# Performance work log

Hardware: AMD Instinct MI355X
Metric: run time of the kernel (lower is better)

The kernel has to match this reference:

```python
import jax, jax.numpy as jnp
import numpy as np

EMB = 256
VOCAB = 50000
STEPS = 100  # max extra decode iterations after the first (output rows = 101)
BN_EPS = 1e-5


def setup_inputs() -> dict:
    key = jax.random.key(0)
    ks = jax.random.split(key, 10)
    s = 0.05
    return {
        "board": jax.random.normal(ks[0], (19, 19), jnp.float32),
        "conv_w": jax.random.normal(ks[1], (1, 1, 3, 3), jnp.float32) * s,
        "conv_b": jnp.zeros((1,), jnp.float32),
        "bn_gamma": jnp.ones((1,), jnp.float32),
        "bn_beta": jnp.zeros((1,), jnp.float32),
        "p": jnp.ones((8,), jnp.float32),
        "W_lin": jax.random.normal(ks[2], (EMB, 361), jnp.float32) * s,
        "b_lin": jnp.zeros((EMB,), jnp.float32),
        "W_ih": jax.random.normal(ks[3], (4 * EMB, EMB), jnp.float32) * s,
        "b_ih": jnp.zeros((4 * EMB,), jnp.float32),
        "W_hh": jax.random.normal(ks[4], (4 * EMB, EMB), jnp.float32) * s,
        "b_hh": jnp.zeros((4 * EMB,), jnp.float32),
        "W_dec": jax.random.normal(ks[5], (VOCAB, EMB), jnp.float32) * s,
        "b_dec": jnp.zeros((VOCAB,), jnp.float32),
    }


def reference(board, conv_w, conv_b, bn_gamma, bn_beta, p,
              W_lin, b_lin, W_ih, b_ih, W_hh, b_hh, W_dec, b_dec):
    # --- shared conv + batchnorm (training-mode stats), all 8 "layers" share weights ---
    def conv_bn(x):  # x: [1,1,19,19]
        y = jax.lax.conv_general_dilated(x, conv_w, (1, 1), 'SAME') + conv_b.reshape(1, 1, 1, 1)
        mu = y.mean()
        var = jnp.mean((y - mu) ** 2)  # biased var over N,H,W (C=1)
        return bn_gamma[0] * (y - mu) * jax.lax.rsqrt(var + BN_EPS) + bn_beta[0]

    relu = jax.nn.relu
    x = board.reshape(1, 1, 19, 19)
    d1 = relu(p[0] * conv_bn(x))
    d2 = d1
    for i in (1, 3, 5):  # fixed structural unroll (residual pairs)
        d1 = relu(p[i] * conv_bn(d1))
        d1 = d2 = relu(p[i + 1] * conv_bn(d1) + d2)
    d1 = relu(conv_bn(d1))  # cnn_list[7], no scalar

    feat = W_lin @ d1.reshape(361) + b_lin  # [EMB]

    # --- LSTMCell (PyTorch gate order i,f,g,o) ---
    def cell(x_in, h, c):
        gates = W_ih @ x_in + b_ih + W_hh @ h + b_hh  # [4*EMB]
        i, f, g, o = jnp.split(gates, 4)
        c2 = jax.nn.sigmoid(f) * c + jax.nn.sigmoid(i) * jnp.tanh(g)
        h2 = jax.nn.sigmoid(o) * jnp.tanh(c2)
        return h2, c2

    zeros = jnp.zeros((EMB,), feat.dtype)
    h, c = cell(feat, zeros, zeros)
    logit0 = W_dec @ h + b_dec  # [VOCAB]

    # (original breaks early on argmax==3; max output rows = 101)
    def step(carry, _):
        h, c = carry
        h2, c2 = cell(h, h, c)
        return (h2, c2), W_dec @ h2 + b_dec

    _, logits = jax.lax.scan(step, (h, c), None, length=STEPS)  # [STEPS, VOCAB]
    out = jax.nn.relu(jnp.concatenate([logit0[None, :], logits], axis=0))  # [101, VOCAB]
    return out
```

## Files before the change

kernel.cpp:

```cpp
#include <hip/hip_runtime.h>

typedef _Float16 v2h __attribute__((ext_vector_type(2)));
typedef _Float16 v8h __attribute__((ext_vector_type(8)));
typedef float v4f __attribute__((ext_vector_type(4)));

#define EMB 256
#define VOCAB 50000
#define NSTEP 101

__device__ __forceinline__ float sigf(float x) {
    return 1.f / (1.f + __expf(-x));
}
__device__ __forceinline__ float tanhf_(float x) {
    float e = __expf(2.f * fabsf(x));
    float th = 1.f - 2.f / (e + 1.f);
    return copysignf(th, x);
}
__device__ __forceinline__ float fdot2_(v2h a, v2h b, float c) {
    return __builtin_amdgcn_fdot2(a, b, c, false);
}

__global__ __launch_bounds__(384) void k_conv(
        const float* __restrict__ board, const float* __restrict__ conv_w,
        const float* __restrict__ conv_b, const float* __restrict__ gamma,
        const float* __restrict__ beta, const float* __restrict__ p,
        float* __restrict__ d1_out) {
    __shared__ float cur[361];
    __shared__ float red1[8], red2[8];
    __shared__ float stats[2];
    const int t = threadIdx.x;
    const bool act = t < 361;
    const int r = t / 19, c = t % 19;
    float w[9];
#pragma unroll
    for (int k = 0; k < 9; ++k) w[k] = conv_w[k];
    const float cb = conv_b[0], ga = gamma[0], be = beta[0];
    float scales[8] = {p[0], p[1], p[2], p[3], p[4], p[5], p[6], 1.f};
    const int mode[8] = {2, 0, 1, 0, 1, 0, 1, 0};
    if (act) cur[t] = board[t];
    float d2r = 0.f;
    __syncthreads();
#pragma unroll
    for (int it = 0; it < 8; ++it) {
        float y = 0.f;
        if (act) {
#pragma unroll
            for (int di = 0; di < 3; ++di)
#pragma unroll
                for (int dj = 0; dj < 3; ++dj) {
                    int rr = r + di - 1, cc2 = c + dj - 1;
                    if (rr >= 0 && rr < 19 && cc2 >= 0 && cc2 < 19)
                        y += cur[rr * 19 + cc2] * w[di * 3 + dj];
                }
            y += cb;
        }
        float s1 = y, s2 = y * y;
        for (int m = 32; m; m >>= 1) {
            s1 += __shfl_xor(s1, m);
            s2 += __shfl_xor(s2, m);
        }
        const int wv = t >> 6;
        if ((t & 63) == 0) { red1[wv] = s1; red2[wv] = s2; }
        __syncthreads();
        if (t == 0) {
            float a = 0.f, b2 = 0.f;
            for (int i = 0; i < 6; ++i) { a += red1[i]; b2 += red2[i]; }
            float mu = a / 361.f;
            float var = b2 / 361.f - mu * mu;
            stats[0] = mu;
            stats[1] = rsqrtf(var + 1e-5f);
        }
        __syncthreads();
        float mu = stats[0], rs = stats[1];
        float v = ga * (y - mu) * rs + be;
        v *= scales[it];
        if (mode[it] == 1) v += d2r;
        v = fmaxf(v, 0.f);
        if (mode[it] != 0) d2r = v;
        if (act) cur[t] = v;
        __syncthreads();
    }
    if (act) d1_out[t] = cur[t];
}

__global__ __launch_bounds__(256) void k_prep(
        const float* __restrict__ Wlin, const float* __restrict__ blin,
        const float* __restrict__ d1,
        const float* __restrict__ Wih, const float* __restrict__ bih,
        const float* __restrict__ Whh, const float* __restrict__ bhh,
        float* __restrict__ feat, _Float16* __restrict__ wsum,
        float* __restrict__ bsum) {
    const int b = blockIdx.x, t = threadIdx.x;
    if (b < 16) {
        const int r = b * 16 + (t >> 4), kc = t & 15;
        const int k0 = kc * 23, k1 = (k0 + 23 < 361) ? k0 + 23 : 361;
        const float* wrow = Wlin + r * 361;
        float acc = 0.f;
        for (int k = k0; k < k1; ++k) acc += wrow[k] * d1[k];
        for (int m = 1; m < 16; m <<= 1) acc += __shfl_xor(acc, m);
        if (kc == 0) feat[r] = acc + blin[r];
    } else if (b < 80) {
        const int base = (b - 16) * 4096 + t;
#pragma unroll
        for (int i = 0; i < 16; ++i) {
            int idx = base + i * 256;
            wsum[idx] = (_Float16)(Wih[idx] + Whh[idx]);
        }
    } else {
        for (int i = t; i < 1024; i += 256) bsum[i] = bih[i] + bhh[i];
    }
}

__global__ __launch_bounds__(256) void k_gates0(
        const float* __restrict__ Wih, const float* __restrict__ feat,
        const float* __restrict__ bih, const float* __restrict__ bhh,
        float* __restrict__ gates0) {
    const int r = blockIdx.x * 16 + (threadIdx.x >> 4), kc = threadIdx.x & 15;
    const float* wrow = Wih + r * 256 + kc * 16;
    const float* f = feat + kc * 16;
    float acc = 0.f;
#pragma unroll
    for (int k = 0; k < 16; ++k) acc += wrow[k] * f[k];
    for (int m = 1; m < 16; m <<= 1) acc += __shfl_xor(acc, m);
    if (kc == 0) gates0[r] = acc + bih[r] + bhh[r];
}

__global__ __launch_bounds__(512, 2) void k_lstm(
        const _Float16* __restrict__ wsum, const float* __restrict__ bsum,
        const float* __restrict__ gates0, _Float16* __restrict__ Hg) {
    extern __shared__ char smem[];
    _Float16* Wl = (_Float16*)smem;
    _Float16* hbuf = (_Float16*)(smem + 131072);
    float* part = (float*)(smem + 131584);
    const int t = threadIdx.x;
    const int idx = t & 255;
    const int half = t >> 8;
    const int kbase = half * 128;
    const int sw = (t & 15) << 4;

    v2h wr[4][48];
#pragma unroll
    for (int j = 0; j < 4; ++j) {
        const _Float16* src = wsum + (idx + 256 * j) * 256 + kbase;
#pragma unroll
        for (int q = 0; q < 12; ++q) {
            float4 fv = *(const float4*)(src + q * 8);
            const v2h* vp = (const v2h*)&fv;
            wr[j][q * 4 + 0] = vp[0];
            wr[j][q * 4 + 1] = vp[1];
            wr[j][q * 4 + 2] = vp[2];
            wr[j][q * 4 + 3] = vp[3];
        }
    }
#pragma unroll
    for (int j = 0; j < 4; ++j) {
        const _Float16* src = wsum + (idx + 256 * j) * 256 + kbase + 96;
#pragma unroll
        for (int cc = 0; cc < 4; ++cc) {
            float4 fv = *(const float4*)(src + cc * 8);
            const int c = j * 4 + cc;
            *(float4*)((char*)Wl + t * 256 + ((c * 16) ^ sw)) = fv;
        }
    }
    const float bs0 = bsum[idx], bs1 = bsum[idx + 256];
    const float bs2 = bsum[idx + 512], bs3 = bsum[idx + 768];
    float cst = 0.f;
    if (half == 0) {
        float gi = gates0[idx], gg = gates0[idx + 512], go = gates0[idx + 768];
        cst = sigf(gi) * tanhf_(gg);
        float h = sigf(go) * tanhf_(cst);
        hbuf[idx] = (_Float16)h;
        Hg[idx] = (_Float16)h;
    }
    __syncthreads();

    for (int step = 1; step <= 100; ++step) {
        float acc[4];
        acc[0] = 0.f; acc[1] = 0.f; acc[2] = 0.f; acc[3] = 0.f;
        const v2h* hp = ((const v2h*)hbuf) + half * 64;
#pragma unroll
        for (int q = 0; q < 12; ++q) {
            float4 hv = *(const float4*)(hp + q * 4);
            const v2h* h4 = (const v2h*)&hv;
#pragma unroll
            for (int j = 0; j < 4; ++j) {
#pragma unroll
                for (int u = 0; u < 4; ++u)
                    acc[j] = fdot2_(wr[j][q * 4 + u], h4[u], acc[j]);
            }
        }
#pragma unroll
        for (int cc = 0; cc < 4; ++cc) {
            float4 hv = *(const float4*)(hp + 48 + cc * 4);
            const v2h* h4 = (const v2h*)&hv;
#pragma unroll
            for (int j = 0; j < 4; ++j) {
                const int c = j * 4 + cc;
                float4 wv = *(const float4*)((const char*)Wl + t * 256 + ((c * 16) ^ sw));
                const v2h* w4 = (const v2h*)&wv;
#pragma unroll
                for (int u = 0; u < 4; ++u)
                    acc[j] = fdot2_(w4[u], h4[u], acc[j]);
            }
        }
        if (half == 1) {
            part[0 * 256 + idx] = acc[0];
            part[1 * 256 + idx] = acc[1];
            part[2 * 256 + idx] = acc[2];
            part[3 * 256 + idx] = acc[3];
        }
        __syncthreads();
        if (half == 0) {
            float gi = acc[0] + part[0 * 256 + idx] + bs0;
            float gf = acc[1] + part[1 * 256 + idx] + bs1;
            float gg = acc[2] + part[2 * 256 + idx] + bs2;
            float go = acc[3] + part[3 * 256 + idx] + bs3;
            cst = sigf(gf) * cst + sigf(gi) * tanhf_(gg);
            float h = sigf(go) * tanhf_(cst);
            hbuf[idx] = (_Float16)h;
            Hg[step * 256 + idx] = (_Float16)h;
        }
        __syncthreads();
    }
}

__global__ __launch_bounds__(256) void k_gemm(
        const float* __restrict__ Wdec, const float* __restrict__ bdec,
        const _Float16* __restrict__ Hg, float* __restrict__ out) {
    __shared__ _Float16 Hl[112 * 264];
    const int t = threadIdx.x;
    float4 z; z.x = 0.f; z.y = 0.f; z.z = 0.f; z.w = 0.f;
    for (int i = t; i < 3696; i += 256) ((float4*)Hl)[i] = z;
    __syncthreads();
    for (int i = t; i < 101 * 32; i += 256) {
        int row = i >> 5, kc = i & 31;
        float4 v = ((const float4*)Hg)[i];
        *(float4*)(Hl + row * 264 + kc * 8) = v;
    }
    __syncthreads();

    const int l = t & 63, wv = t >> 6;
    const int mrow = blockIdx.x * 64 + wv * 16 + (l & 15);
    const int mcl = (mrow < VOCAB) ? mrow : (VOCAB - 1);
    const float* arow = Wdec + (size_t)mcl * 256 + ((l >> 4) << 3);
    const _Float16* brow = Hl + (l & 15) * 264 + ((l >> 4) << 3);

    v4f acc[7];
#pragma unroll
    for (int nt = 0; nt < 7; ++nt) {
#pragma unroll
        for (int j = 0; j < 4; ++j) acc[nt][j] = 0.f;
    }
#pragma unroll
    for (int ks = 0; ks < 8; ++ks) {
        float4 a0 = *(const float4*)(arow + ks * 32);
        float4 a1 = *(const float4*)(arow + ks * 32 + 4);
        v8h af;
        af[0] = (_Float16)a0.x; af[1] = (_Float16)a0.y;
        af[2] = (_Float16)a0.z; af[3] = (_Float16)a0.w;
        af[4] = (_Float16)a1.x; af[5] = (_Float16)a1.y;
        af[6] = (_Float16)a1.z; af[7] = (_Float16)a1.w;
#pragma unroll
        for (int nt = 0; nt < 7; ++nt) {
            v8h bf = *(const v8h*)(brow + nt * 16 * 264 + ks * 32);
            acc[nt] = __builtin_amdgcn_mfma_f32_16x16x32_f16(af, bf, acc[nt], 0, 0, 0);
        }
    }
    const int rowq = blockIdx.x * 64 + wv * 16 + ((l >> 4) << 2);
    if (rowq < VOCAB) {
        float4 bd = *(const float4*)(bdec + rowq);
#pragma unroll
        for (int nt = 0; nt < 7; ++nt) {
            int tt = nt * 16 + (l & 15);
            if (tt <= 100) {
                float4 v;
                v.x = fmaxf(acc[nt][0] + bd.x, 0.f);
                v.y = fmaxf(acc[nt][1] + bd.y, 0.f);
                v.z = fmaxf(acc[nt][2] + bd.z, 0.f);
                v.w = fmaxf(acc[nt][3] + bd.w, 0.f);
                *(float4*)(out + (size_t)tt * VOCAB + rowq) = v;
            }
        }
    }
}

extern "C" void kernel_launch(void* const* d_in, const int* in_sizes, int n_in,
                              void* d_out, int out_size, void* d_ws, size_t ws_size,
                              hipStream_t stream) {
    const float* board  = (const float*)d_in[0];
    const float* conv_w = (const float*)d_in[1];
    const float* conv_b = (const float*)d_in[2];
    const float* bn_g   = (const float*)d_in[3];
    const float* bn_b   = (const float*)d_in[4];
    const float* p      = (const float*)d_in[5];
    const float* Wlin   = (const float*)d_in[6];
    const float* blin   = (const float*)d_in[7];
    const float* Wih    = (const float*)d_in[8];
    const float* bih    = (const float*)d_in[9];
    const float* Whh    = (const float*)d_in[10];
    const float* bhh    = (const float*)d_in[11];
    const float* Wdec   = (const float*)d_in[12];
    const float* bdec   = (const float*)d_in[13];
    float* out = (float*)d_out;
    char* ws = (char*)d_ws;

    _Float16* wsum  = (_Float16*)(ws);
    _Float16* Hg    = (_Float16*)(ws + 524288);
    float* d1       = (float*)(ws + 576512);
    float* feat     = (float*)(ws + 578560);
    float* gates0   = (float*)(ws + 579584);
    float* bsum     = (float*)(ws + 583680);

    k_conv<<<1, 384, 0, stream>>>(board, conv_w, conv_b, bn_g, bn_b, p, d1);
    k_prep<<<81, 256, 0, stream>>>(Wlin, blin, d1, Wih, bih, Whh, bhh, feat, wsum, bsum);
    k_gates0<<<64, 256, 0, stream>>>(Wih, feat, bih, bhh, gates0);
    k_lstm<<<1, 512, 135680, stream>>>(wsum, bsum, gates0, Hg);
    k_gemm<<<782, 256, 0, stream>>>(Wdec, bdec, Hg, out);
}
```

Before: 304.3 us.

## Overlap W_dec fp16 conversion with LSTM recurrence and fuse prep kernels

Merges the conv/BN, feature, gates0 and weight-sum prep into one kernel and so cuts the launch count from five to three. The LSTM kernel is launched with 128 extra blocks that convert W_dec to fp16 in workspace while block 0 runs the serial recurrence. The recurrence is re-split across 4 threads per gate-row group, reduced with shuffles instead of shared-memory partials, and uses double-buffered h so one barrier per step is dropped. The GEMM then reads half the weight bytes as fp16. This depends on the workspace being large enough and falls back to the fp32 GEMM otherwise. The converter blocks may compete with the recurrence for bandwidth or compute units.

```diff
diff --git a/kernel.cpp b/kernel.cpp
--- a/kernel.cpp
+++ b/kernel.cpp
@@ -1,12 +1,12 @@
 #include <hip/hip_runtime.h>
 
 typedef _Float16 v2h __attribute__((ext_vector_type(2)));
+typedef _Float16 v4h __attribute__((ext_vector_type(4)));
 typedef _Float16 v8h __attribute__((ext_vector_type(8)));
 typedef float v4f __attribute__((ext_vector_type(4)));
 
 #define EMB 256
 #define VOCAB 50000
-#define NSTEP 101
 
 __device__ __forceinline__ float sigf(float x) {
     return 1.f / (1.f + __expf(-x));
@@ -20,182 +20,205 @@
     return __builtin_amdgcn_fdot2(a, b, c, false);
 }
 
-__global__ __launch_bounds__(384) void k_conv(
+__global__ __launch_bounds__(512) void k_pre(
         const float* __restrict__ board, const float* __restrict__ conv_w,
         const float* __restrict__ conv_b, const float* __restrict__ gamma,
         const float* __restrict__ beta, const float* __restrict__ p,
-        float* __restrict__ d1_out) {
-    __shared__ float cur[361];
-    __shared__ float red1[8], red2[8];
-    __shared__ float stats[2];
-    const int t = threadIdx.x;
-    const bool act = t < 361;
-    const int r = t / 19, c = t % 19;
-    float w[9];
-#pragma unroll
-    for (int k = 0; k < 9; ++k) w[k] = conv_w[k];
-    const float cb = conv_b[0], ga = gamma[0], be = beta[0];
-    float scales[8] = {p[0], p[1], p[2], p[3], p[4], p[5], p[6], 1.f};
-    const int mode[8] = {2, 0, 1, 0, 1, 0, 1, 0};
-    if (act) cur[t] = board[t];
-    float d2r = 0.f;
-    __syncthreads();
-#pragma unroll
-    for (int it = 0; it < 8; ++it) {
-        float y = 0.f;
-        if (act) {
-#pragma unroll
-            for (int di = 0; di < 3; ++di)
-#pragma unroll
-                for (int dj = 0; dj < 3; ++dj) {
-                    int rr = r + di - 1, cc2 = c + dj - 1;
-                    if (rr >= 0 && rr < 19 && cc2 >= 0 && cc2 < 19)
-                        y += cur[rr * 19 + cc2] * w[di * 3 + dj];
-                }
-            y += cb;
-        }
-        float s1 = y, s2 = y * y;
-        for (int m = 32; m; m >>= 1) {
-            s1 += __shfl_xor(s1, m);
-            s2 += __shfl_xor(s2, m);
-        }
-        const int wv = t >> 6;
-        if ((t & 63) == 0) { red1[wv] = s1; red2[wv] = s2; }
-        __syncthreads();
-        if (t == 0) {
-            float a = 0.f, b2 = 0.f;
-            for (int i = 0; i < 6; ++i) { a += red1[i]; b2 += red2[i]; }
-            float mu = a / 361.f;
-            float var = b2 / 361.f - mu * mu;
-            stats[0] = mu;
-            stats[1] = rsqrtf(var + 1e-5f);
-        }
-        __syncthreads();
-        float mu = stats[0], rs = stats[1];
-        float v = ga * (y - mu) * rs + be;
-        v *= scales[it];
-        if (mode[it] == 1) v += d2r;
-        v = fmaxf(v, 0.f);
-        if (mode[it] != 0) d2r = v;
-        if (act) cur[t] = v;
-        __syncthreads();
-    }
-    if (act) d1_out[t] = cur[t];
-}
-
-__global__ __launch_bounds__(256) void k_prep(
         const float* __restrict__ Wlin, const float* __restrict__ blin,
-        const float* __restrict__ d1,
         const float* __restrict__ Wih, const float* __restrict__ bih,
         const float* __restrict__ Whh, const float* __restrict__ bhh,
-        float* __restrict__ feat, _Float16* __restrict__ wsum,
-        float* __restrict__ bsum) {
+        _Float16* __restrict__ wsum, float* __restrict__ bsum,
+        float* __restrict__ gates0) {
+    __shared__ float cur[361];
+    __shared__ float feat_s[256];
+    __shared__ float red1[8], red2[8], stats[2];
     const int b = blockIdx.x, t = threadIdx.x;
-    if (b < 16) {
-        const int r = b * 16 + (t >> 4), kc = t & 15;
-        const int k0 = kc * 23, k1 = (k0 + 23 < 361) ? k0 + 23 : 361;
-        const float* wrow = Wlin + r * 361;
-        float acc = 0.f;
-        for (int k = k0; k < k1; ++k) acc += wrow[k] * d1[k];
-        for (int m = 1; m < 16; m <<= 1) acc += __shfl_xor(acc, m);
-        if (kc == 0) feat[r] = acc + blin[r];
-    } else if (b < 80) {
-        const int base = (b - 16) * 4096 + t;
-#pragma unroll
-        for (int i = 0; i < 16; ++i) {
-            int idx = base + i * 256;
+    if (b == 0) {
+        const bool act = t < 361;
+        const int r = t / 19, c = t % 19;
+        float w[9];
+#pragma unroll
+        for (int k = 0; k < 9; ++k) w[k] = conv_w[k];
+        const float cb = conv_b[0], ga = gamma[0], be = beta[0];
+        float scales[8] = {p[0], p[1], p[2], p[3], p[4], p[5], p[6], 1.f};
+        const int mode[8] = {2, 0, 1, 0, 1, 0, 1, 0};
+        if (act) cur[t] = board[t];
+        float d2r = 0.f;
+        __syncthreads();
+#pragma unroll
+        for (int it = 0; it < 8; ++it) {
+            float y = 0.f;
+            if (act) {
+#pragma unroll
+                for (int di = 0; di < 3; ++di)
+#pragma unroll
+                    for (int dj = 0; dj < 3; ++dj) {
+                        int rr = r + di - 1, cc2 = c + dj - 1;
+                        if (rr >= 0 && rr < 19 && cc2 >= 0 && cc2 < 19)
+                            y += cur[rr * 19 + cc2] * w[di * 3 + dj];
+                    }
+                y += cb;
+            }
+            float s1 = y, s2 = y * y;
+            for (int m = 32; m; m >>= 1) {
+                s1 += __shfl_xor(s1, m);
+                s2 += __shfl_xor(s2, m);
+            }
+            const int wv = t >> 6;
+            if ((t & 63) == 0) { red1[wv] = s1; red2[wv] = s2; }
+            __syncthreads();
+            if (t == 0) {
+                float a = 0.f, b2 = 0.f;
+                for (int i = 0; i < 8; ++i) { a += red1[i]; b2 += red2[i]; }
+                float mu = a / 361.f;
+                float var = b2 / 361.f - mu * mu;
+                stats[0] = mu;
+                stats[1] = rsqrtf(var + 1e-5f);
+            }
+            __syncthreads();
+            float mu = stats[0], rs = stats[1];
+            float v = ga * (y - mu) * rs + be;
+            v *= scales[it];
+            if (mode[it] == 1) v += d2r;
+            v = fmaxf(v, 0.f);
+            if (mode[it] != 0) d2r = v;
+            if (act) cur[t] = v;
+            __syncthreads();
+        }
+        {
+            const int fr = t >> 1, fh = t & 1;
+            const int k0 = fh ? 184 : 0, k1 = fh ? 361 : 184;
+            const float* wrow = Wlin + fr * 361;
+            float acc = 0.f;
+            for (int k = k0; k < k1; ++k) acc += wrow[k] * cur[k];
+            acc += __shfl_xor(acc, 1);
+            if (fh == 0) feat_s[fr] = acc + blin[fr];
+        }
+        __syncthreads();
+#pragma unroll
+        for (int rr = 0; rr < 2; ++rr) {
+            const int row = t + rr * 512;
+            const float4* wr4 = (const float4*)(Wih + row * 256);
+            float a = 0.f;
+            for (int k = 0; k < 64; ++k) {
+                float4 wv = wr4[k];
+                float4 fv = *(const float4*)(feat_s + k * 4);
+                a += wv.x * fv.x + wv.y * fv.y + wv.z * fv.z + wv.w * fv.w;
+            }
+            gates0[row] = a + bih[row] + bhh[row];
+        }
+    } else if (b <= 8) {
+        const int base = (b - 1) * 32768 + t;
+#pragma unroll
+        for (int i = 0; i < 64; ++i) {
+            int idx = base + i * 512;
             wsum[idx] = (_Float16)(Wih[idx] + Whh[idx]);
         }
     } else {
-        for (int i = t; i < 1024; i += 256) bsum[i] = bih[i] + bhh[i];
-    }
-}
-
-__global__ __launch_bounds__(256) void k_gates0(
-        const float* __restrict__ Wih, const float* __restrict__ feat,
-        const float* __restrict__ bih, const float* __restrict__ bhh,
-        float* __restrict__ gates0) {
-    const int r = blockIdx.x * 16 + (threadIdx.x >> 4), kc = threadIdx.x & 15;
-    const float* wrow = Wih + r * 256 + kc * 16;
-    const float* f = feat + kc * 16;
-    float acc = 0.f;
-#pragma unroll
-    for (int k = 0; k < 16; ++k) acc += wrow[k] * f[k];
-    for (int m = 1; m < 16; m <<= 1) acc += __shfl_xor(acc, m);
-    if (kc == 0) gates0[r] = acc + bih[r] + bhh[r];
+        for (int i = t; i < 1024; i += 512) bsum[i] = bih[i] + bhh[i];
+    }
 }
 
 __global__ __launch_bounds__(512, 2) void k_lstm(
         const _Float16* __restrict__ wsum, const float* __restrict__ bsum,
-        const float* __restrict__ gates0, _Float16* __restrict__ Hg) {
+        const float* __restrict__ gates0, _Float16* __restrict__ Hg,
+        const float* __restrict__ Wdec, _Float16* __restrict__ wdh) {
+    if (blockIdx.x != 0) {
+        const float4* src = (const float4*)Wdec;
+        const int gid = (blockIdx.x - 1) * 512 + threadIdx.x;
+        for (int i = gid; i < 3200000; i += 65536) {
+            float4 v = src[i];
+            v4h o;
+            o[0] = (_Float16)v.x; o[1] = (_Float16)v.y;
+            o[2] = (_Float16)v.z; o[3] = (_Float16)v.w;
+            *(v4h*)(wdh + (size_t)i * 4) = o;
+        }
+        return;
+    }
     extern __shared__ char smem[];
     _Float16* Wl = (_Float16*)smem;
-    _Float16* hbuf = (_Float16*)(smem + 131072);
-    float* part = (float*)(smem + 131584);
+    char* hb0 = smem + 131072;
     const int t = threadIdx.x;
-    const int idx = t & 255;
-    const int half = t >> 8;
-    const int kbase = half * 128;
+    const int g = t >> 2;
+    const int ks = t & 3;
+    const int k0 = ks * 64;
     const int sw = (t & 15) << 4;
 
-    v2h wr[4][48];
-#pragma unroll
-    for (int j = 0; j < 4; ++j) {
-        const _Float16* src = wsum + (idx + 256 * j) * 256 + kbase;
-#pragma unroll
-        for (int q = 0; q < 12; ++q) {
-            float4 fv = *(const float4*)(src + q * 8);
+    int rows[8];
+#pragma unroll
+    for (int j = 0; j < 4; ++j) { rows[j] = g + 256 * j; rows[j + 4] = g + 128 + 256 * j; }
+
+    v2h wr[8][24];
+#pragma unroll
+    for (int j = 0; j < 8; ++j) {
+        const _Float16* src = wsum + rows[j] * 256 + k0;
+#pragma unroll
+        for (int q6 = 0; q6 < 6; ++q6) {
+            float4 fv = *(const float4*)(src + q6 * 8);
             const v2h* vp = (const v2h*)&fv;
-            wr[j][q * 4 + 0] = vp[0];
-            wr[j][q * 4 + 1] = vp[1];
-            wr[j][q * 4 + 2] = vp[2];
-            wr[j][q * 4 + 3] = vp[3];
-        }
-    }
-#pragma unroll
-    for (int j = 0; j < 4; ++j) {
-        const _Float16* src = wsum + (idx + 256 * j) * 256 + kbase + 96;
-#pragma unroll
-        for (int cc = 0; cc < 4; ++cc) {
+            wr[j][q6 * 4 + 0] = vp[0];
+            wr[j][q6 * 4 + 1] = vp[1];
+            wr[j][q6 * 4 + 2] = vp[2];
+            wr[j][q6 * 4 + 3] = vp[3];
+        }
+    }
+#pragma unroll
+    for (int j = 0; j < 8; ++j)
+#pragma unroll
+        for (int q = 0; q < 24; ++q)
+            asm volatile("" : "+v"(wr[j][q]));
+
+#pragma unroll
+    for (int j = 0; j < 8; ++j) {
+        const _Float16* src = wsum + rows[j] * 256 + k0 + 48;
+#pragma unroll
+        for (int cc = 0; cc < 2; ++cc) {
             float4 fv = *(const float4*)(src + cc * 8);
-            const int c = j * 4 + cc;
+            const int c = j * 2 + cc;
             *(float4*)((char*)Wl + t * 256 + ((c * 16) ^ sw)) = fv;
         }
     }
-    const float bs0 = bsum[idx], bs1 = bsum[idx + 256];
-    const float bs2 = bsum[idx + 512], bs3 = bsum[idx + 768];
+    float bsv[8];
+#pragma unroll
+    for (int j = 0; j < 8; ++j) bsv[j] = bsum[rows[j]];
+
+    const int cell = (ks == 0) ? g : g + 128;
+    const int haddr = ((cell >> 6) * 144) + ((cell & 63) * 2);
     float cst = 0.f;
-    if (half == 0) {
-        float gi = gates0[idx], gg = gates0[idx + 512], go = gates0[idx + 768];
+    if (ks < 2) {
+        float gi = gates0[cell], gg = gates0[cell + 512], go = gates0[cell + 768];
         cst = sigf(gi) * tanhf_(gg);
         float h = sigf(go) * tanhf_(cst);
-        hbuf[idx] = (_Float16)h;
-        Hg[idx] = (_Float16)h;
+        *(_Float16*)(hb0 + haddr) = (_Float16)h;
+        Hg[cell] = (_Float16)h;
     }
     __syncthreads();
 
     for (int step = 1; step <= 100; ++step) {
-        float acc[4];
-        acc[0] = 0.f; acc[1] = 0.f; acc[2] = 0.f; acc[3] = 0.f;
-        const v2h* hp = ((const v2h*)hbuf) + half * 64;
-#pragma unroll
-        for (int q = 0; q < 12; ++q) {
-            float4 hv = *(const float4*)(hp + q * 4);
+        const char* hr = hb0 + ((step + 1) & 1) * 576;
+        char* hw = hb0 + (step & 1) * 576;
+        const char* hsl = hr + ks * 144;
+        float acc[8];
+#pragma unroll
+        for (int j = 0; j < 8; ++j) acc[j] = 0.f;
+#pragma unroll
+        for (int q = 0; q < 6; ++q) {
+            float4 hv = *(const float4*)(hsl + q * 16);
             const v2h* h4 = (const v2h*)&hv;
 #pragma unroll
-            for (int j = 0; j < 4; ++j) {
+            for (int j = 0; j < 8; ++j) {
 #pragma unroll
                 for (int u = 0; u < 4; ++u)
                     acc[j] = fdot2_(wr[j][q * 4 + u], h4[u], acc[j]);
             }
         }
 #pragma unroll
-        for (int cc = 0; cc < 4; ++cc) {
-            float4 hv = *(const float4*)(hp + 48 + cc * 4);
+        for (int cc = 0; cc < 2; ++cc) {
+            float4 hv = *(const float4*)(hsl + 96 + cc * 16);
             const v2h* h4 = (const v2h*)&hv;
 #pragma unroll
-            for (int j = 0; j < 4; ++j) {
-                const int c = j * 4 + cc;
+            for (int j = 0; j < 8; ++j) {
+                const int c = j * 2 + cc;
                 float4 wv = *(const float4*)((const char*)Wl + t * 256 + ((c * 16) ^ sw));
                 const v2h* w4 = (const v2h*)&wv;
 #pragma unroll
@@ -203,28 +226,88 @@
                     acc[j] = fdot2_(w4[u], h4[u], acc[j]);
             }
         }
-        if (half == 1) {
-            part[0 * 256 + idx] = acc[0];
-            part[1 * 256 + idx] = acc[1];
-            part[2 * 256 + idx] = acc[2];
-            part[3 * 256 + idx] = acc[3];
-        }
-        __syncthreads();
-        if (half == 0) {
-            float gi = acc[0] + part[0 * 256 + idx] + bs0;
-            float gf = acc[1] + part[1 * 256 + idx] + bs1;
-            float gg = acc[2] + part[2 * 256 + idx] + bs2;
-            float go = acc[3] + part[3 * 256 + idx] + bs3;
+#pragma unroll
+        for (int j = 0; j < 8; ++j) {
+            acc[j] += __shfl_xor(acc[j], 1);
+            acc[j] += __shfl_xor(acc[j], 2);
+        }
+        if (ks < 2) {
+            float gi, gf, gg, go;
+            if (ks == 0) {
+                gi = acc[0] + bsv[0]; gf = acc[1] + bsv[1];
+                gg = acc[2] + bsv[2]; go = acc[3] + bsv[3];
+            } else {
+                gi = acc[4] + bsv[4]; gf = acc[5] + bsv[5];
+                gg = acc[6] + bsv[6]; go = acc[7] + bsv[7];
+            }
             cst = sigf(gf) * cst + sigf(gi) * tanhf_(gg);
             float h = sigf(go) * tanhf_(cst);
-            hbuf[idx] = (_Float16)h;
-            Hg[step * 256 + idx] = (_Float16)h;
+            *(_Float16*)(hw + haddr) = (_Float16)h;
+            Hg[step * 256 + cell] = (_Float16)h;
         }
         __syncthreads();
     }
 }
 
-__global__ __launch_bounds__(256) void k_gemm(
+__global__ __launch_bounds__(256) void k_gemm_f16(
+        const _Float16* __restrict__ wdh, const float* __restrict__ bdec,
+        const _Float16* __restrict__ Hg, float* __restrict__ out) {
+    __shared__ _Float16 Hl[112 * 264];
+    const int t = threadIdx.x;
+    {
+        float4 z; z.x = 0.f; z.y = 0.f; z.z = 0.f; z.w = 0.f;
+        for (int i = t; i < 11 * 33; i += 256) {
+            int row = 101 + i / 33, kc = i % 33;
+            *(float4*)(Hl + row * 264 + kc * 8) = z;
+        }
+    }
+    for (int i = t; i < 101 * 32; i += 256) {
+        int row = i >> 5, kc = i & 31;
+        float4 v = ((const float4*)Hg)[i];
+        *(float4*)(Hl + row * 264 + kc * 8) = v;
+    }
+    __syncthreads();
+
+    const int l = t & 63, wv = t >> 6;
+    const int mrow = blockIdx.x * 64 + wv * 16 + (l & 15);
+    const int mcl = (mrow < VOCAB) ? mrow : (VOCAB - 1);
+    const _Float16* arow = wdh + (size_t)mcl * 256 + ((l >> 4) << 3);
+    const _Float16* brow = Hl + (l & 15) * 264 + ((l >> 4) << 3);
+
+    v4f acc[7];
+#pragma unroll
+    for (int nt = 0; nt < 7; ++nt) {
+#pragma unroll
+        for (int j = 0; j < 4; ++j) acc[nt][j] = 0.f;
+    }
+#pragma unroll
+    for (int ks = 0; ks < 8; ++ks) {
+        v8h af = *(const v8h*)(arow + ks * 32);
+#pragma unroll
+        for (int nt = 0; nt < 7; ++nt) {
+            v8h bf = *(const v8h*)(brow + nt * 16 * 264 + ks * 32);
+            acc[nt] = __builtin_amdgcn_mfma_f32_16x16x32_f16(af, bf, acc[nt], 0, 0, 0);
+        }
+    }
+    const int rowq = blockIdx.x * 64 + wv * 16 + ((l >> 4) << 2);
+    if (rowq < VOCAB) {
+        float4 bd = *(const float4*)(bdec + rowq);
+#pragma unroll
+        for (int nt = 0; nt < 7; ++nt) {
+            int tt = nt * 16 + (l & 15);
+            if (tt <= 100) {
+                float4 v;
+                v.x = fmaxf(acc[nt][0] + bd.x, 0.f);
+                v.y = fmaxf(acc[nt][1] + bd.y, 0.f);
+                v.z = fmaxf(acc[nt][2] + bd.z, 0.f);
+                v.w = fmaxf(acc[nt][3] + bd.w, 0.f);
+                *(float4*)(out + (size_t)tt * VOCAB + rowq) = v;
+            }
+        }
+    }
+}
+
+__global__ __launch_bounds__(256) void k_gemm_f32(
         const float* __restrict__ Wdec, const float* __restrict__ bdec,
         const _Float16* __restrict__ Hg, float* __restrict__ out) {
     __shared__ _Float16 Hl[112 * 264];
@@ -238,13 +321,11 @@
         *(float4*)(Hl + row * 264 + kc * 8) = v;
     }
     __syncthreads();
-
     const int l = t & 63, wv = t >> 6;
     const int mrow = blockIdx.x * 64 + wv * 16 + (l & 15);
     const int mcl = (mrow < VOCAB) ? mrow : (VOCAB - 1);
     const float* arow = Wdec + (size_t)mcl * 256 + ((l >> 4) << 3);
     const _Float16* brow = Hl + (l & 15) * 264 + ((l >> 4) << 3);
-
     v4f acc[7];
 #pragma unroll
     for (int nt = 0; nt < 7; ++nt) {
@@ -306,14 +387,18 @@
 
     _Float16* wsum  = (_Float16*)(ws);
     _Float16* Hg    = (_Float16*)(ws + 524288);
-    float* d1       = (float*)(ws + 576512);
-    float* feat     = (float*)(ws + 578560);
-    float* gates0   = (float*)(ws + 579584);
-    float* bsum     = (float*)(ws + 583680);
-
-    k_conv<<<1, 384, 0, stream>>>(board, conv_w, conv_b, bn_g, bn_b, p, d1);
-    k_prep<<<81, 256, 0, stream>>>(Wlin, blin, d1, Wih, bih, Whh, bhh, feat, wsum, bsum);
-    k_gates0<<<64, 256, 0, stream>>>(Wih, feat, bih, bhh, gates0);
-    k_lstm<<<1, 512, 135680, stream>>>(wsum, bsum, gates0, Hg);
-    k_gemm<<<782, 256, 0, stream>>>(Wdec, bdec, Hg, out);
-}
+    float* gates0   = (float*)(ws + 576000);
+    float* bsum     = (float*)(ws + 580096);
+    _Float16* wdh   = (_Float16*)(ws + 584192);
+    const size_t NEED = 584192ull + 25600000ull;
+    const bool fit = ws_size >= NEED;
+
+    k_pre<<<10, 512, 0, stream>>>(board, conv_w, conv_b, bn_g, bn_b, p,
+                                  Wlin, blin, Wih, bih, Whh, bhh,
+                                  wsum, bsum, gates0);
+    k_lstm<<<fit ? 129 : 1, 512, 132224, stream>>>(wsum, bsum, gates0, Hg, Wdec, wdh);
+    if (fit)
+        k_gemm_f16<<<782, 256, 0, stream>>>(wdh, bdec, Hg, out);
+    else
+        k_gemm_f32<<<782, 256, 0, stream>>>(Wdec, bdec, Hg, out);
+}
```

New measurement: 523.7 us. +72.1%, slower.

## Restructure LSTM recurrence to 256 threads with shuffle reduction and double-buffered h

Applied to the files above, without the earlier changes.

The single-block LSTM kernel now uses 256 threads, each computing partial dot products for 16 gate rows over a 64-wide K slice. Partials are combined with intra-quad shuffles instead of shared-memory partials, and h is double-buffered. This removes one of the two barriers per step and the shared-memory partial exchange, cutting per-step latency in the serial recurrence. In exchange each thread carries more registers (16x24 weight pairs) and does more serial FMA work per step, which risks spills or longer compute per step.

```diff
diff --git a/kernel.cpp b/kernel.cpp
--- a/kernel.cpp
+++ b/kernel.cpp
@@ -6,7 +6,6 @@
 
 #define EMB 256
 #define VOCAB 50000
-#define NSTEP 101
 
 __device__ __forceinline__ float sigf(float x) {
     return 1.f / (1.f + __expf(-x));
@@ -125,101 +124,119 @@
     if (kc == 0) gates0[r] = acc + bih[r] + bhh[r];
 }
 
-__global__ __launch_bounds__(512, 2) void k_lstm(
+__global__ __launch_bounds__(256, 1) void k_lstm(
         const _Float16* __restrict__ wsum, const float* __restrict__ bsum,
         const float* __restrict__ gates0, _Float16* __restrict__ Hg) {
     extern __shared__ char smem[];
     _Float16* Wl = (_Float16*)smem;
-    _Float16* hbuf = (_Float16*)(smem + 131072);
-    float* part = (float*)(smem + 131584);
+    char* hb0 = smem + 131072;
     const int t = threadIdx.x;
-    const int idx = t & 255;
-    const int half = t >> 8;
-    const int kbase = half * 128;
+    const int g = t >> 2;
+    const int ks = t & 3;
+    const int k0 = ks * 64;
     const int sw = (t & 15) << 4;
 
-    v2h wr[4][48];
-#pragma unroll
-    for (int j = 0; j < 4; ++j) {
-        const _Float16* src = wsum + (idx + 256 * j) * 256 + kbase;
-#pragma unroll
-        for (int q = 0; q < 12; ++q) {
-            float4 fv = *(const float4*)(src + q * 8);
-            const v2h* vp = (const v2h*)&fv;
-            wr[j][q * 4 + 0] = vp[0];
-            wr[j][q * 4 + 1] = vp[1];
-            wr[j][q * 4 + 2] = vp[2];
-            wr[j][q * 4 + 3] = vp[3];
-        }
-    }
-#pragma unroll
-    for (int j = 0; j < 4; ++j) {
-        const _Float16* src = wsum + (idx + 256 * j) * 256 + kbase + 96;
-#pragma unroll
-        for (int cc = 0; cc < 4; ++cc) {
-            float4 fv = *(const float4*)(src + cc * 8);
-            const int c = j * 4 + cc;
-            *(float4*)((char*)Wl + t * 256 + ((c * 16) ^ sw)) = fv;
-        }
-    }
-    const float bs0 = bsum[idx], bs1 = bsum[idx + 256];
-    const float bs2 = bsum[idx + 512], bs3 = bsum[idx + 768];
+    v2h wr[16][24];
+#pragma unroll
+    for (int m = 0; m < 4; ++m) {
+#pragma unroll
+        for (int j = 0; j < 4; ++j) {
+            const int row = (g + 64 * m) + 256 * j;
+            const _Float16* src = wsum + row * 256 + k0;
+            const int rr = m * 4 + j;
+#pragma unroll
+            for (int q6 = 0; q6 < 6; ++q6) {
+                float4 fv = *(const float4*)(src + q6 * 8);
+                const v2h* vp = (const v2h*)&fv;
+                wr[rr][q6 * 4 + 0] = vp[0];
+                wr[rr][q6 * 4 + 1] = vp[1];
+                wr[rr][q6 * 4 + 2] = vp[2];
+                wr[rr][q6 * 4 + 3] = vp[3];
+            }
+        }
+    }
+#pragma unroll
+    for (int rr = 0; rr < 16; ++rr)
+#pragma unroll
+        for (int q = 0; q < 24; ++q)
+            asm("" : "+v"(wr[rr][q]));
+
+#pragma unroll
+    for (int m = 0; m < 4; ++m) {
+#pragma unroll
+        for (int j = 0; j < 4; ++j) {
+            const int row = (g + 64 * m) + 256 * j;
+            const _Float16* src = wsum + row * 256 + k0 + 48;
+            const int rr = m * 4 + j;
+#pragma unroll
+            for (int cc = 0; cc < 2; ++cc) {
+                float4 fv = *(const float4*)(src + cc * 8);
+                const int c = rr * 2 + cc;
+                *(float4*)((char*)Wl + t * 512 + ((c * 16) ^ sw)) = fv;
+            }
+        }
+    }
+    float bsv[4];
+    const int cellT = g + 64 * ks;
+#pragma unroll
+    for (int j = 0; j < 4; ++j) bsv[j] = bsum[cellT + 256 * j];
+
     float cst = 0.f;
-    if (half == 0) {
-        float gi = gates0[idx], gg = gates0[idx + 512], go = gates0[idx + 768];
+    {
+        float gi = gates0[cellT], gg = gates0[cellT + 512], go = gates0[cellT + 768];
         cst = sigf(gi) * tanhf_(gg);
         float h = sigf(go) * tanhf_(cst);
-        hbuf[idx] = (_Float16)h;
-        Hg[idx] = (_Float16)h;
+        *(_Float16*)(hb0 + cellT * 2) = (_Float16)h;
+        Hg[cellT] = (_Float16)h;
     }
     __syncthreads();
 
     for (int step = 1; step <= 100; ++step) {
-        float acc[4];
-        acc[0] = 0.f; acc[1] = 0.f; acc[2] = 0.f; acc[3] = 0.f;
-        const v2h* hp = ((const v2h*)hbuf) + half * 64;
-#pragma unroll
-        for (int q = 0; q < 12; ++q) {
-            float4 hv = *(const float4*)(hp + q * 4);
+        const char* hr = hb0 + ((step + 1) & 1) * 512;
+        char* hw = hb0 + (step & 1) * 512;
+        const char* hsl = hr + ks * 128;
+        float acc[16];
+#pragma unroll
+        for (int rr = 0; rr < 16; ++rr) acc[rr] = 0.f;
+#pragma unroll
+        for (int q = 0; q < 6; ++q) {
+            float4 hv = *(const float4*)(hsl + q * 16);
             const v2h* h4 = (const v2h*)&hv;
 #pragma unroll
-            for (int j = 0; j < 4; ++j) {
+            for (int rr = 0; rr < 16; ++rr) {
 #pragma unroll
                 for (int u = 0; u < 4; ++u)
-                    acc[j] = fdot2_(wr[j][q * 4 + u], h4[u], acc[j]);
-            }
-        }
-#pragma unroll
-        for (int cc = 0; cc < 4; ++cc) {
-            float4 hv = *(const float4*)(hp + 48 + cc * 4);
+                    acc[rr] = fdot2_(wr[rr][q * 4 + u], h4[u], acc[rr]);
+            }
+        }
+#pragma unroll
+        for (int cc = 0; cc < 2; ++cc) {
+            float4 hv = *(const float4*)(hsl + 96 + cc * 16);
             const v2h* h4 = (const v2h*)&hv;
 #pragma unroll
-            for (int j = 0; j < 4; ++j) {
-                const int c = j * 4 + cc;
-                float4 wv = *(const float4*)((const char*)Wl + t * 256 + ((c * 16) ^ sw));
+            for (int rr = 0; rr < 16; ++rr) {
+                const int c = rr * 2 + cc;
+                float4 wv = *(const float4*)((const char*)Wl + t * 512 + ((c * 16) ^ sw));
                 const v2h* w4 = (const v2h*)&wv;
 #pragma unroll
                 for (int u = 0; u < 4; ++u)
-                    acc[j] = fdot2_(w4[u], h4[u], acc[j]);
-            }
-        }
-        if (half == 1) {
-            part[0 * 256 + idx] = acc[0];
-            part[1 * 256 + idx] = acc[1];
-            part[2 * 256 + idx] = acc[2];
-            part[3 * 256 + idx] = acc[3];
-        }
-        __syncthreads();
-        if (half == 0) {
-            float gi = acc[0] + part[0 * 256 + idx] + bs0;
-            float gf = acc[1] + part[1 * 256 + idx] + bs1;
-            float gg = acc[2] + part[2 * 256 + idx] + bs2;
-            float go = acc[3] + part[3 * 256 + idx] + bs3;
-            cst = sigf(gf) * cst + sigf(gi) * tanhf_(gg);
-            float h = sigf(go) * tanhf_(cst);
-            hbuf[idx] = (_Float16)h;
-            Hg[step * 256 + idx] = (_Float16)h;
-        }
+                    acc[rr] = fdot2_(w4[u], h4[u], acc[rr]);
+            }
+        }
+#pragma unroll
+        for (int rr = 0; rr < 16; ++rr) {
+            acc[rr] += __shfl_xor(acc[rr], 1);
+            acc[rr] += __shfl_xor(acc[rr], 2);
+        }
+        float gi = ks == 0 ? acc[0] : ks == 1 ? acc[4] : ks == 2 ? acc[8]  : acc[12];
+        float gf = ks == 0 ? acc[1] : ks == 1 ? acc[5] : ks == 2 ? acc[9]  : acc[13];
+        float gg = ks == 0 ? acc[2] : ks == 1 ? acc[6] : ks == 2 ? acc[10] : acc[14];
+        float go = ks == 0 ? acc[3] : ks == 1 ? acc[7] : ks == 2 ? acc[11] : acc[15];
+        gi += bsv[0]; gf += bsv[1]; gg += bsv[2]; go += bsv[3];
+        cst = sigf(gf) * cst + sigf(gi) * tanhf_(gg);
+        float h = sigf(go) * tanhf_(cst);
+        *(_Float16*)(hw + cellT * 2) = (_Float16)h;
+        Hg[step * 256 + cellT] = (_Float16)h;
         __syncthreads();
     }
 }
@@ -314,6 +331,6 @@
     k_conv<<<1, 384, 0, stream>>>(board, conv_w, conv_b, bn_g, bn_b, p, d1);
     k_prep<<<81, 256, 0, stream>>>(Wlin, blin, d1, Wih, bih, Whh, bhh, feat, wsum, bsum);
     k_gates0<<<64, 256, 0, stream>>>(Wih, feat, bih, bhh, gates0);
-    k_lstm<<<1, 512, 135680, stream>>>(wsum, bsum, gates0, Hg);
+    k_lstm<<<1, 256, 132096, stream>>>(wsum, bsum, gates0, Hg);
     k_gemm<<<782, 256, 0, stream>>>(Wdec, bdec, Hg, out);
 }
```

New measurement: 492.4 us. +61.9%, slower.
